# Optimization experiments

Measured on AMD Instinct MI355X. Metric: run time of the kernel, lower is better.

Reference implementation:

```python
import jax, jax.numpy as jnp
import numpy as np

N, M, F = 16384, 16384, 512
NUM_BATCHES = 16


def setup_inputs() -> dict:
    key = jax.random.key(0)
    k1, k2, k3, k4 = jax.random.split(key, 4)
    H_q = jax.random.normal(k1, (N, F), dtype=jnp.float32)
    H_c = jax.random.normal(k2, (M, F), dtype=jnp.float32)
    batch_q = jnp.sort(jax.random.randint(k3, (N,), 0, NUM_BATCHES, dtype=jnp.int64))
    batch_c = jnp.sort(jax.random.randint(k4, (M,), 0, NUM_BATCHES, dtype=jnp.int64))
    return {"H_q": H_q, "H_c": H_c, "batch_q": batch_q, "batch_c": batch_c}


def reference(H_q, H_c, batch_q, batch_c):
    # scores: [n, m] dense dot-product similarity
    scores = jnp.matmul(H_q, H_c.T)
    # mask[i, j] = True iff query i and candidate j belong to the same batch element
    mask = batch_q[:, None] == batch_c[None, :]
    out = jnp.where(mask, scores, -jnp.inf)
    return out, mask
```

## Files before the change

kernel.cpp:

```cpp
#include <hip/hip_runtime.h>
#include <hip/hip_bf16.h>
#include <math.h>


#define BM 128
#define BN 128
#define NEG_BIG (-3.3895313892515355e+38f)

typedef float    f32x4  __attribute__((ext_vector_type(4)));
typedef unsigned u32x4  __attribute__((ext_vector_type(4)));
typedef short    short8 __attribute__((ext_vector_type(8)));

__device__ __forceinline__ unsigned pk2(float a, float b) {
    unsigned ua = __builtin_bit_cast(unsigned, a);
    unsigned ub = __builtin_bit_cast(unsigned, b);
    return (ub & 0xFFFF0000u) | (ua >> 16);
}

__global__ __launch_bounds__(256) void cvt_kernel(
    const float* __restrict__ Hq, const float* __restrict__ Hc,
    unsigned short* __restrict__ q_bf, unsigned short* __restrict__ c_bf,
    long long nq, long long ntot)
{
    const long long ng = ntot >> 3;
    for (long long g = (long long)blockIdx.x * 256 + threadIdx.x; g < ng;
         g += (long long)gridDim.x * 256) {
        const long long base = g << 3;
        const float* src;
        unsigned short* dst;
        if (base < nq) { src = Hq + base;        dst = q_bf + base; }
        else           { src = Hc + (base - nq); dst = c_bf + (base - nq); }
        f32x4 a = *(const f32x4*)(src);
        f32x4 b = *(const f32x4*)(src + 4);
        u32x4 p = (u32x4){pk2(a[0],a[1]), pk2(a[2],a[3]),
                          pk2(b[0],b[1]), pk2(b[2],b[3])};
        *(u32x4*)dst = p;
    }
}

template <int USE_BF>
__global__ __launch_bounds__(256) void dot_tile_kernel(
    const float* __restrict__ Hq, const float* __restrict__ Hc,
    const unsigned short* __restrict__ Hq_bf, const unsigned short* __restrict__ Hc_bf,
    const int* __restrict__ bq, const int* __restrict__ bc,
    float* __restrict__ out, float* __restrict__ mask_out,
    int M, int F, int ntx, int write_mask)
{
    const int t   = threadIdx.x;
    const int bid = blockIdx.x;
    const int i0  = (bid / ntx) * BM;
    const int j0  = (bid % ntx) * BN;

    if (!(bq[i0] <= bc[j0 + BN - 1] && bc[j0] <= bq[i0 + BM - 1])) {
        const f32x4 m4 = (f32x4){NEG_BIG, NEG_BIG, NEG_BIG, NEG_BIG};
        const f32x4 z4 = (f32x4){0.f, 0.f, 0.f, 0.f};
        #pragma unroll
        for (int v = 0; v < 16; ++v) {
            const int idx = t + v * 256;
            const int r   = idx >> 5;
            const int c4  = idx & 31;
            const size_t off = (size_t)(i0 + r) * M + j0 + c4 * 4;
            *(f32x4*)(out + off) = m4;
            if (write_mask) *(f32x4*)(mask_out + off) = z4;
        }
        return;
    }

    __shared__ short Abf[128 * 32];
    __shared__ short Bbf[128 * 32];
    __shared__ int bql[BM];
    __shared__ int bcl[BN];

    if (t < BM) bql[t] = bq[i0 + t];
    else        bcl[t - BM] = bc[j0 + (t - BM)];

    f32x4 acc[4][4];
    #pragma unroll
    for (int a = 0; a < 4; ++a)
        #pragma unroll
        for (int b = 0; b < 4; ++b) acc[a][b] = (f32x4){0.f, 0.f, 0.f, 0.f};

    const int l   = t & 63;
    const int wid = t >> 6;
    const int wr  = wid >> 1;
    const int wc  = wid & 1;
    const int lg  = l >> 4;
    const int lm  = l & 15;

    const int sr   = t >> 1;
    const int half = t & 1;
    const int swW = ((sr >> 1) & 3) << 4;
    const int wb0 = sr * 64 + half * 32;
    const int swR = ((lm >> 1) & 3) << 4;

    char* Ab = (char*)Abf;
    char* Bb = (char*)Bbf;

    const int nks = F >> 5;

    const float* aptrf = Hq + (size_t)(i0 + sr) * F + half * 16;
    const float* bptrf = Hc + (size_t)(j0 + sr) * F + half * 16;
    const char*  aptrb = (const char*)Hq_bf + (size_t)(i0 + sr) * F * 2 + half * 32;
    const char*  bptrb = (const char*)Hc_bf + (size_t)(j0 + sr) * F * 2 + half * 32;

    for (int ks = 0; ks < nks; ++ks) {
        u32x4 pa0, pa1, pb0, pb1;
        if (USE_BF) {
            pa0 = *(const u32x4*)(aptrb + ks * 64);
            pa1 = *(const u32x4*)(aptrb + ks * 64 + 16);
            pb0 = *(const u32x4*)(bptrb + ks * 64);
            pb1 = *(const u32x4*)(bptrb + ks * 64 + 16);
        } else {
            const int k0 = ks * 32;
            f32x4 a0 = *(const f32x4*)(aptrf + k0);
            f32x4 a1 = *(const f32x4*)(aptrf + k0 + 4);
            f32x4 a2 = *(const f32x4*)(aptrf + k0 + 8);
            f32x4 a3 = *(const f32x4*)(aptrf + k0 + 12);
            f32x4 b0 = *(const f32x4*)(bptrf + k0);
            f32x4 b1 = *(const f32x4*)(bptrf + k0 + 4);
            f32x4 b2 = *(const f32x4*)(bptrf + k0 + 8);
            f32x4 b3 = *(const f32x4*)(bptrf + k0 + 12);
            pa0 = (u32x4){pk2(a0[0],a0[1]), pk2(a0[2],a0[3]), pk2(a1[0],a1[1]), pk2(a1[2],a1[3])};
            pa1 = (u32x4){pk2(a2[0],a2[1]), pk2(a2[2],a2[3]), pk2(a3[0],a3[1]), pk2(a3[2],a3[3])};
            pb0 = (u32x4){pk2(b0[0],b0[1]), pk2(b0[2],b0[3]), pk2(b1[0],b1[1]), pk2(b1[2],b1[3])};
            pb1 = (u32x4){pk2(b2[0],b2[1]), pk2(b2[2],b2[3]), pk2(b3[0],b3[1]), pk2(b3[2],b3[3])};
        }
        __syncthreads();
        *(u32x4*)(Ab + ((wb0     ) ^ swW)) = pa0;
        *(u32x4*)(Ab + ((wb0 + 16) ^ swW)) = pa1;
        *(u32x4*)(Bb + ((wb0     ) ^ swW)) = pb0;
        *(u32x4*)(Bb + ((wb0 + 16) ^ swW)) = pb1;
        __syncthreads();
        short8 af[4], bf[4];
        #pragma unroll
        for (int m = 0; m < 4; ++m) {
            const int arow = wr * 64 + m * 16 + lm;
            af[m] = *(const short8*)(Ab + arow * 64 + ((lg * 16) ^ swR));
            const int brow = wc * 64 + m * 16 + lm;
            bf[m] = *(const short8*)(Bb + brow * 64 + ((lg * 16) ^ swR));
        }
        #pragma unroll
        for (int m = 0; m < 4; ++m)
            #pragma unroll
            for (int n = 0; n < 4; ++n)
                acc[m][n] = __builtin_amdgcn_mfma_f32_16x16x32_bf16(
                    af[m], bf[n], acc[m][n], 0, 0, 0);
    }

    #pragma unroll
    for (int m = 0; m < 4; ++m) {
        #pragma unroll
        for (int v = 0; v < 4; ++v) {
            const int rit = wr * 64 + m * 16 + lg * 4 + v;
            const int bqv = bql[rit];
            const size_t rowoff = (size_t)(i0 + rit) * M + j0;
            #pragma unroll
            for (int n = 0; n < 4; ++n) {
                const int cit = wc * 64 + n * 16 + lm;
                const bool eq = (bqv == bcl[cit]);
                out[rowoff + cit] = eq ? acc[m][n][v] : NEG_BIG;
                if (write_mask) mask_out[rowoff + cit] = eq ? 1.0f : 0.0f;
            }
        }
    }
}

extern "C" void kernel_launch(void* const* d_in, const int* in_sizes, int n_in,
                              void* d_out, int out_size, void* d_ws, size_t ws_size,
                              hipStream_t stream) {
    const float* Hq = (const float*)d_in[0];
    const float* Hc = (const float*)d_in[1];
    const int*   bq = (const int*)d_in[2];
    const int*   bc = (const int*)d_in[3];

    const int N = in_sizes[2];
    const int M = in_sizes[3];
    const int F = in_sizes[0] / N;

    float* out = (float*)d_out;
    const long long NM = (long long)N * M;
    const int write_mask = ((long long)out_size >= 2 * NM) ? 1 : 0;
    float* mask_out = out + NM;

    const long long nq = (long long)N * F;
    const long long nc = (long long)M * F;
    const int use_bf = (ws_size >= (size_t)(nq + nc) * 2) ? 1 : 0;

    unsigned short* q_bf = (unsigned short*)d_ws;
    unsigned short* c_bf = q_bf + nq;

    const int nty = N / BM;
    const int ntx = M / BN;

    if (use_bf) {
        cvt_kernel<<<2048, 256, 0, stream>>>(Hq, Hc, q_bf, c_bf, nq, nq + nc);
        dot_tile_kernel<1><<<nty * ntx, 256, 0, stream>>>(
            Hq, Hc, q_bf, c_bf, bq, bc, out, mask_out, M, F, ntx, write_mask);
    } else {
        dot_tile_kernel<0><<<nty * ntx, 256, 0, stream>>>(
            Hq, Hc, q_bf, c_bf, bq, bc, out, mask_out, M, F, ntx, write_mask);
    }
}
```

Before: 458.2 us.

## Split masked fill into row-span fill blocks and write only matching tile entries

The conversion kernel now also computes, for each query row, the candidate index span sharing its batch via binary search. A new fused kernel dedicates a fixed set of blocks to filling the out and mask arrays row-segment-wise with the sentinel/zero values outside each row's span, while the MFMA tile blocks return early for non-overlapping tiles and write only matching entries. This aims to make the fill fully coalesced 1024-wide row segments and to cut the per-element masked stores in compute tiles. It adds shape restrictions (square, power-of-two segments) with a fallback path, and leaves some dead leftover variables in the fill code.

New measurement: 635.3 us. +38.7%, slower.

```diff
diff --git a/kernel.cpp b/kernel.cpp
--- a/kernel.cpp
+++ b/kernel.cpp
@@ -5,12 +5,23 @@
 
 #define BM 128
 #define BN 128
+#define NFILL 1536
 #define NEG_BIG (-3.3895313892515355e+38f)
 
 typedef float    f32x4  __attribute__((ext_vector_type(4)));
 typedef unsigned u32x4  __attribute__((ext_vector_type(4)));
 typedef short    short8 __attribute__((ext_vector_type(8)));
 
+__device__ __forceinline__ int lbound(const int* __restrict__ a, int n, int v) {
+    int lo = 0, hi = n;
+    while (lo < hi) { int mid = (lo + hi) >> 1; if (a[mid] < v) lo = mid + 1; else hi = mid; }
+    return lo;
+}
+__device__ __forceinline__ int ubound(const int* __restrict__ a, int n, int v) {
+    int lo = 0, hi = n;
+    while (lo < hi) { int mid = (lo + hi) >> 1; if (a[mid] <= v) lo = mid + 1; else hi = mid; }
+    return lo;
+}
 __device__ __forceinline__ unsigned pk2(float a, float b) {
     unsigned ua = __builtin_bit_cast(unsigned, a);
     unsigned ub = __builtin_bit_cast(unsigned, b);
@@ -19,12 +30,18 @@
 
 __global__ __launch_bounds__(256) void cvt_kernel(
     const float* __restrict__ Hq, const float* __restrict__ Hc,
+    const int* __restrict__ bq, const int* __restrict__ bc,
     unsigned short* __restrict__ q_bf, unsigned short* __restrict__ c_bf,
-    long long nq, long long ntot)
+    int* __restrict__ spans, int N, int M, long long nq, long long ntot)
 {
+    const long long gid0 = (long long)blockIdx.x * 256 + threadIdx.x;
+    if (gid0 < N) {
+        const int b = bq[(int)gid0];
+        spans[2 * gid0]     = lbound(bc, M, b);
+        spans[2 * gid0 + 1] = ubound(bc, M, b);
+    }
     const long long ng = ntot >> 3;
-    for (long long g = (long long)blockIdx.x * 256 + threadIdx.x; g < ng;
-         g += (long long)gridDim.x * 256) {
+    for (long long g = gid0; g < ng; g += (long long)gridDim.x * 256) {
         const long long base = g << 3;
         const float* src;
         unsigned short* dst;
@@ -32,16 +49,143 @@
         else           { src = Hc + (base - nq); dst = c_bf + (base - nq); }
         f32x4 a = *(const f32x4*)(src);
         f32x4 b = *(const f32x4*)(src + 4);
-        u32x4 p = (u32x4){pk2(a[0],a[1]), pk2(a[2],a[3]),
-                          pk2(b[0],b[1]), pk2(b[2],b[3])};
-        *(u32x4*)dst = p;
-    }
-}
-
-template <int USE_BF>
-__global__ __launch_bounds__(256) void dot_tile_kernel(
+        *(u32x4*)dst = (u32x4){pk2(a[0],a[1]), pk2(a[2],a[3]),
+                               pk2(b[0],b[1]), pk2(b[2],b[3])};
+    }
+}
+
+__global__ __launch_bounds__(256) void main_kernel(
+    const unsigned short* __restrict__ Hq_bf, const unsigned short* __restrict__ Hc_bf,
+    const int* __restrict__ bq, const int* __restrict__ bc,
+    const int* __restrict__ spans,
+    float* __restrict__ out, float* __restrict__ mask_out,
+    int M, int F, int ntx, int write_mask, int seg_shift)
+{
+    const int t   = threadIdx.x;
+    const int bid = blockIdx.x;
+
+    if (bid < NFILL) {
+        const int spr_mask = (1 << seg_shift) - 1;
+        const long long nseg_out = (long long)(ntx * BN / 1024) == 0 ? 0 : 0;
+        const int rows = M;
+        (void)rows; (void)nseg_out;
+        const long long spo = (long long)M << (seg_shift - (seg_shift));
+        (void)spo;
+        const long long nsegO = ((long long)M * M) >> 10;
+        const long long nsegT = 2 * nsegO;
+        for (long long seg = bid; seg < nsegT; seg += NFILL) {
+            const bool isOut = (seg < nsegO) || !write_mask;
+            const long long s = (seg < nsegO) ? seg : seg - nsegO;
+            if (!isOut && !write_mask) continue;
+            float* base = isOut ? out : mask_out;
+            const float fv = isOut ? NEG_BIG : 0.0f;
+            const int r  = (int)(s >> seg_shift);
+            const int c0 = ((int)s & spr_mask) << 10;
+            const int lo = spans[2 * r], hi = spans[2 * r + 1];
+            const int c  = c0 + t * 4;
+            float* p = base + (size_t)r * M + c;
+            if (c + 4 <= lo || c >= hi) {
+                *(f32x4*)p = (f32x4){fv, fv, fv, fv};
+            } else if (c < lo || c + 4 > hi) {
+                #pragma unroll
+                for (int j = 0; j < 4; ++j) {
+                    const int cc = c + j;
+                    if (cc < lo || cc >= hi) p[j] = fv;
+                }
+            }
+        }
+        return;
+    }
+
+    const int cid = bid - NFILL;
+    const int i0  = (cid / ntx) * BM;
+    const int j0  = (cid % ntx) * BN;
+
+    if (!(bq[i0] <= bc[j0 + BN - 1] && bc[j0] <= bq[i0 + BM - 1])) return;
+
+    __shared__ short Abf[128 * 32];
+    __shared__ short Bbf[128 * 32];
+    __shared__ int bql[BM];
+    __shared__ int bcl[BN];
+
+    if (t < BM) bql[t] = bq[i0 + t];
+    else        bcl[t - BM] = bc[j0 + (t - BM)];
+
+    f32x4 acc[4][4];
+    #pragma unroll
+    for (int a = 0; a < 4; ++a)
+        #pragma unroll
+        for (int b = 0; b < 4; ++b) acc[a][b] = (f32x4){0.f, 0.f, 0.f, 0.f};
+
+    const int l   = t & 63;
+    const int wid = t >> 6;
+    const int wr  = wid >> 1;
+    const int wc  = wid & 1;
+    const int lg  = l >> 4;
+    const int lm  = l & 15;
+
+    const int sr   = t >> 1;
+    const int half = t & 1;
+    const int swW = ((sr >> 1) & 3) << 4;
+    const int wb0 = sr * 64 + half * 32;
+    const int swR = ((lm >> 1) & 3) << 4;
+
+    char* Ab = (char*)Abf;
+    char* Bb = (char*)Bbf;
+
+    const int nks = F >> 5;
+
+    const char* aptrb = (const char*)Hq_bf + (size_t)(i0 + sr) * F * 2 + half * 32;
+    const char* bptrb = (const char*)Hc_bf + (size_t)(j0 + sr) * F * 2 + half * 32;
+
+    for (int ks = 0; ks < nks; ++ks) {
+        u32x4 pa0 = *(const u32x4*)(aptrb + ks * 64);
+        u32x4 pa1 = *(const u32x4*)(aptrb + ks * 64 + 16);
+        u32x4 pb0 = *(const u32x4*)(bptrb + ks * 64);
+        u32x4 pb1 = *(const u32x4*)(bptrb + ks * 64 + 16);
+        __syncthreads();
+        *(u32x4*)(Ab + ((wb0     ) ^ swW)) = pa0;
+        *(u32x4*)(Ab + ((wb0 + 16) ^ swW)) = pa1;
+        *(u32x4*)(Bb + ((wb0     ) ^ swW)) = pb0;
+        *(u32x4*)(Bb + ((wb0 + 16) ^ swW)) = pb1;
+        __syncthreads();
+        short8 af[4], bf[4];
+        #pragma unroll
+        for (int m = 0; m < 4; ++m) {
+            const int arow = wr * 64 + m * 16 + lm;
+            af[m] = *(const short8*)(Ab + arow * 64 + ((lg * 16) ^ swR));
+            const int brow = wc * 64 + m * 16 + lm;
+            bf[m] = *(const short8*)(Bb + brow * 64 + ((lg * 16) ^ swR));
+        }
+        #pragma unroll
+        for (int m = 0; m < 4; ++m)
+            #pragma unroll
+            for (int n = 0; n < 4; ++n)
+                acc[m][n] = __builtin_amdgcn_mfma_f32_16x16x32_bf16(
+                    af[m], bf[n], acc[m][n], 0, 0, 0);
+    }
+
+    #pragma unroll
+    for (int m = 0; m < 4; ++m) {
+        #pragma unroll
+        for (int v = 0; v < 4; ++v) {
+            const int rit = wr * 64 + m * 16 + lg * 4 + v;
+            const int bqv = bql[rit];
+            const size_t rowoff = (size_t)(i0 + rit) * M + j0;
+            #pragma unroll
+            for (int n = 0; n < 4; ++n) {
+                const int cit = wc * 64 + n * 16 + lm;
+                if (bqv == bcl[cit]) {
+                    out[rowoff + cit] = acc[m][n][v];
+                    if (write_mask) mask_out[rowoff + cit] = 1.0f;
+                }
+            }
+        }
+    }
+}
+
+__global__ __launch_bounds__(256) void fallback_kernel(
     const float* __restrict__ Hq, const float* __restrict__ Hc,
-    const unsigned short* __restrict__ Hq_bf, const unsigned short* __restrict__ Hc_bf,
     const int* __restrict__ bq, const int* __restrict__ bc,
     float* __restrict__ out, float* __restrict__ mask_out,
     int M, int F, int ntx, int write_mask)
@@ -95,36 +239,25 @@
 
     char* Ab = (char*)Abf;
     char* Bb = (char*)Bbf;
-
     const int nks = F >> 5;
 
     const float* aptrf = Hq + (size_t)(i0 + sr) * F + half * 16;
     const float* bptrf = Hc + (size_t)(j0 + sr) * F + half * 16;
-    const char*  aptrb = (const char*)Hq_bf + (size_t)(i0 + sr) * F * 2 + half * 32;
-    const char*  bptrb = (const char*)Hc_bf + (size_t)(j0 + sr) * F * 2 + half * 32;
 
     for (int ks = 0; ks < nks; ++ks) {
-        u32x4 pa0, pa1, pb0, pb1;
-        if (USE_BF) {
-            pa0 = *(const u32x4*)(aptrb + ks * 64);
-            pa1 = *(const u32x4*)(aptrb + ks * 64 + 16);
-            pb0 = *(const u32x4*)(bptrb + ks * 64);
-            pb1 = *(const u32x4*)(bptrb + ks * 64 + 16);
-        } else {
-            const int k0 = ks * 32;
-            f32x4 a0 = *(const f32x4*)(aptrf + k0);
-            f32x4 a1 = *(const f32x4*)(aptrf + k0 + 4);
-            f32x4 a2 = *(const f32x4*)(aptrf + k0 + 8);
-            f32x4 a3 = *(const f32x4*)(aptrf + k0 + 12);
-            f32x4 b0 = *(const f32x4*)(bptrf + k0);
-            f32x4 b1 = *(const f32x4*)(bptrf + k0 + 4);
-            f32x4 b2 = *(const f32x4*)(bptrf + k0 + 8);
-            f32x4 b3 = *(const f32x4*)(bptrf + k0 + 12);
-            pa0 = (u32x4){pk2(a0[0],a0[1]), pk2(a0[2],a0[3]), pk2(a1[0],a1[1]), pk2(a1[2],a1[3])};
-            pa1 = (u32x4){pk2(a2[0],a2[1]), pk2(a2[2],a2[3]), pk2(a3[0],a3[1]), pk2(a3[2],a3[3])};
-            pb0 = (u32x4){pk2(b0[0],b0[1]), pk2(b0[2],b0[3]), pk2(b1[0],b1[1]), pk2(b1[2],b1[3])};
-            pb1 = (u32x4){pk2(b2[0],b2[1]), pk2(b2[2],b2[3]), pk2(b3[0],b3[1]), pk2(b3[2],b3[3])};
-        }
+        const int k0 = ks * 32;
+        f32x4 a0 = *(const f32x4*)(aptrf + k0);
+        f32x4 a1 = *(const f32x4*)(aptrf + k0 + 4);
+        f32x4 a2 = *(const f32x4*)(aptrf + k0 + 8);
+        f32x4 a3 = *(const f32x4*)(aptrf + k0 + 12);
+        f32x4 b0 = *(const f32x4*)(bptrf + k0);
+        f32x4 b1 = *(const f32x4*)(bptrf + k0 + 4);
+        f32x4 b2 = *(const f32x4*)(bptrf + k0 + 8);
+        f32x4 b3 = *(const f32x4*)(bptrf + k0 + 12);
+        u32x4 pa0 = (u32x4){pk2(a0[0],a0[1]), pk2(a0[2],a0[3]), pk2(a1[0],a1[1]), pk2(a1[2],a1[3])};
+        u32x4 pa1 = (u32x4){pk2(a2[0],a2[1]), pk2(a2[2],a2[3]), pk2(a3[0],a3[1]), pk2(a3[2],a3[3])};
+        u32x4 pb0 = (u32x4){pk2(b0[0],b0[1]), pk2(b0[2],b0[3]), pk2(b1[0],b1[1]), pk2(b1[2],b1[3])};
+        u32x4 pb1 = (u32x4){pk2(b2[0],b2[1]), pk2(b2[2],b2[3]), pk2(b3[0],b3[1]), pk2(b3[2],b3[3])};
         __syncthreads();
         *(u32x4*)(Ab + ((wb0     ) ^ swW)) = pa0;
         *(u32x4*)(Ab + ((wb0 + 16) ^ swW)) = pa1;
@@ -184,20 +317,28 @@
 
     const long long nq = (long long)N * F;
     const long long nc = (long long)M * F;
-    const int use_bf = (ws_size >= (size_t)(nq + nc) * 2) ? 1 : 0;
-
-    unsigned short* q_bf = (unsigned short*)d_ws;
-    unsigned short* c_bf = q_bf + nq;
+    const size_t ws_need = (size_t)2 * N * 4 + (size_t)(nq + nc) * 2;
 
     const int nty = N / BM;
     const int ntx = M / BN;
-
-    if (use_bf) {
-        cvt_kernel<<<2048, 256, 0, stream>>>(Hq, Hc, q_bf, c_bf, nq, nq + nc);
-        dot_tile_kernel<1><<<nty * ntx, 256, 0, stream>>>(
-            Hq, Hc, q_bf, c_bf, bq, bc, out, mask_out, M, F, ntx, write_mask);
+    const int spr = M >> 10;
+
+    const bool ok_shape = (N == M) && (M % 1024 == 0) && (spr > 0) &&
+                          ((spr & (spr - 1)) == 0) && (N % BM == 0) && (M % BN == 0);
+
+    if (ok_shape && ws_size >= ws_need) {
+        int* spans = (int*)d_ws;
+        unsigned short* q_bf = (unsigned short*)((char*)d_ws + (size_t)2 * N * 4);
+        unsigned short* c_bf = q_bf + nq;
+        int seg_shift = 0; while ((1 << seg_shift) < spr) ++seg_shift;
+
+        cvt_kernel<<<2048, 256, 0, stream>>>(Hq, Hc, bq, bc, q_bf, c_bf,
+                                             spans, N, M, nq, nq + nc);
+        main_kernel<<<NFILL + nty * ntx, 256, 0, stream>>>(
+            q_bf, c_bf, bq, bc, spans, out, mask_out,
+            M, F, ntx, write_mask, seg_shift);
     } else {
-        dot_tile_kernel<0><<<nty * ntx, 256, 0, stream>>>(
-            Hq, Hc, q_bf, c_bf, bq, bc, out, mask_out, M, F, ntx, write_mask);
-    }
-}
+        fallback_kernel<<<nty * ntx, 256, 0, stream>>>(
+            Hq, Hc, bq, bc, out, mask_out, M, F, ntx, write_mask);
+    }
+}
```
